# Performance work log

Hardware: AMD Instinct MI355X
Metric: run time of the kernel (lower is better)

The kernel has to match this reference:

```python
import jax, jax.numpy as jnp
import numpy as np

NEG_RATIO = 3.0           # negative_ratio
FALLBACK_NEG = 0.0        # fallback_negative_num
EPS = 1e-6                # eps
LOG_CLAMP = -100.0        # torch BCELoss clamps log to -100


def setup_inputs() -> dict:
    key = jax.random.key(0)
    k1, k2, k3 = jax.random.split(key, 3)
    shape = (32, 640, 640)  # [B, H, W] DBNet-style shrink maps
    # probabilities strictly inside (0,1)
    pred = jax.random.uniform(k1, shape, jnp.float32, 1e-4, 1.0 - 1e-4)
    gt = (jax.random.uniform(k2, shape) < 0.05).astype(jnp.float32)
    mask = (jax.random.uniform(k3, shape) < 0.9).astype(jnp.float32)
    return {"pred": pred, "gt": gt, "mask": mask}


def reference(pred, gt, mask):
    positive = gt * mask
    negative = (1.0 - gt) * mask
    # torch uses int(sum()); masks are binary so sums are integral, floor is exact
    pos_count = jnp.floor(positive.sum())
    neg_total = jnp.floor(negative.sum())
    neg_count = jnp.where(
        pos_count == 0,
        jnp.minimum(neg_total, FALLBACK_NEG),
        jnp.minimum(neg_total, jnp.floor(pos_count * NEG_RATIO)),
    )

    # BCE with torch's log clamp at -100
    log_p = jnp.maximum(jnp.log(pred), LOG_CLAMP)
    log_1mp = jnp.maximum(jnp.log1p(-pred), LOG_CLAMP)
    loss = -(gt * log_p + (1.0 - gt) * log_1mp)

    positive_sum = (loss * positive).sum()

    # hard-negative mining: take the top `neg_count` negative losses.
    # neg_count is data-dependent, so sort descending and mask by rank
    # (jit-compatible, same math as torch.topk(...).sum()).
    neg_loss = (loss * negative).reshape(-1)
    neg_sorted = -jnp.sort(-neg_loss)  # descending
    ranks = jnp.arange(neg_sorted.shape[0], dtype=jnp.float32)
    negative_sum = jnp.where(ranks < neg_count, neg_sorted, 0.0).sum()

    return (positive_sum + negative_sum) / (pos_count + neg_count + EPS)
```

## Files before the change

### kernel.cpp

```cpp
#include <hip/hip_runtime.h>
#include <math.h>


#define NBINS1 4096
#define K1_BLOCKS 1024

struct Ctrl {
  unsigned long long pos_cnt;
  unsigned long long neg_cnt;
  unsigned long long k;
  double pos_sum;
  unsigned B;
  unsigned k_rem;
};

#define LN2F 0.69314718055994530942f

__device__ __forceinline__ float neg_loss_from(float p) {
  return -fmaxf(__log2f(1.0f - p) * LN2F, -100.0f);
}
__device__ __forceinline__ float pos_loss_from(float p) {
  return -fmaxf(__log2f(p) * LN2F, -100.0f);
}

__device__ __forceinline__ double bin_mid(unsigned b) {
  return (double)__uint_as_float((b << 19) | 0x40000u);
}

extern "C" __global__ void __launch_bounds__(256)
k1_hist(const float* __restrict__ pred, const float* __restrict__ gt,
        const float* __restrict__ mask, unsigned* __restrict__ hist1,
        Ctrl* __restrict__ ctrl, int n4, int n) {
  __shared__ unsigned h[NBINS1];
  for (int i = threadIdx.x; i < NBINS1; i += blockDim.x) h[i] = 0u;
  __syncthreads();

  unsigned pc = 0, nc = 0;
  double psum = 0.0;
  const float4* p4 = (const float4*)pred;
  const float4* g4 = (const float4*)gt;
  const float4* m4 = (const float4*)mask;
  int gtid = blockIdx.x * blockDim.x + threadIdx.x;
  int stride = gridDim.x * blockDim.x;

  for (int i = gtid; i < n4; i += stride) {
    float4 pv = p4[i], gv = g4[i], mv = m4[i];
    float pa[4] = {pv.x, pv.y, pv.z, pv.w};
    float ga[4] = {gv.x, gv.y, gv.z, gv.w};
    float ma[4] = {mv.x, mv.y, mv.z, mv.w};
#pragma unroll
    for (int j = 0; j < 4; j++) {
      if (ma[j] != 0.0f) {
        if (ga[j] != 0.0f) {
          pc++; psum += (double)pos_loss_from(pa[j]);
        } else {
          nc++;
          atomicAdd(&h[__float_as_uint(neg_loss_from(pa[j])) >> 19], 1u);
        }
      }
    }
  }
  for (int i = n4 * 4 + gtid; i < n; i += stride) {
    float p = pred[i], g = gt[i], m = mask[i];
    if (m != 0.0f) {
      if (g != 0.0f) { pc++; psum += (double)pos_loss_from(p); }
      else {
        nc++;
        atomicAdd(&h[__float_as_uint(neg_loss_from(p)) >> 19], 1u);
      }
    }
  }

  unsigned long long pcl = pc, ncl = nc;
  for (int off = 32; off > 0; off >>= 1) {
    pcl += __shfl_down(pcl, off);
    ncl += __shfl_down(ncl, off);
    psum += __shfl_down(psum, off);
  }
  __shared__ unsigned long long spc[4], snc[4];
  __shared__ double sps[4];
  int wv = threadIdx.x >> 6, ln = threadIdx.x & 63;
  if (ln == 0) { spc[wv] = pcl; snc[wv] = ncl; sps[wv] = psum; }
  __syncthreads();
  if (threadIdx.x == 0) {
    unsigned long long tp = 0, tn = 0; double ts = 0.0;
    for (int w = 0; w < 4; w++) { tp += spc[w]; tn += snc[w]; ts += sps[w]; }
    atomicAdd(&ctrl->pos_cnt, tp);
    atomicAdd(&ctrl->neg_cnt, tn);
    unsafeAtomicAdd(&ctrl->pos_sum, ts);
  }
  for (int i = threadIdx.x; i < NBINS1; i += blockDim.x) {
    unsigned c = h[i];
    if (c) atomicAdd(&hist1[i], c);
  }
}

extern "C" __global__ void __launch_bounds__(256)
k5_final(const unsigned* __restrict__ hist1, Ctrl* __restrict__ ctrl,
         float* __restrict__ out) {
  const int T = 256, CH = NBINS1 / T;
  __shared__ unsigned long long sarr[T];
  __shared__ unsigned long long sk;
  __shared__ unsigned sB, skrem;
  __shared__ double sred[4];
  int t = threadIdx.x;
  int wv = t >> 6, ln = t & 63;

  unsigned cnt[CH];
  unsigned long long tot = 0;
  for (int j = 0; j < CH; j++) { cnt[j] = hist1[t * CH + j]; tot += cnt[j]; }
  sarr[t] = tot;
  if (t == 0) {
    sB = 0xFFFFFFFFu; skrem = 0u;
    unsigned long long pos = ctrl->pos_cnt, negtot = ctrl->neg_cnt;
    unsigned long long k = 0;
    if (pos > 0) {
      k = pos * 3ull;
      if (k > negtot) k = negtot;
    }
    ctrl->k = k;
    sk = k;
  }
  __syncthreads();
  for (int off = 1; off < T; off <<= 1) {
    unsigned long long v = (t + off < T) ? sarr[t + off] : 0ull;
    __syncthreads();
    sarr[t] += v;
    __syncthreads();
  }
  unsigned long long k = sk;
  if (k > 0) {
    unsigned long long above = sarr[t] - tot;
    if (above < k && sarr[t] >= k) {
      unsigned long long cum = above;
      for (int j = CH - 1; j >= 0; j--) {
        if (cum + (unsigned long long)cnt[j] >= k) {
          sB = (unsigned)(t * CH + j);
          skrem = (unsigned)(k - cum);
          break;
        }
        cum += cnt[j];
      }
    }
  }
  __syncthreads();
  unsigned B = sB;

  double s = 0.0;
  if (B != 0xFFFFFFFFu) {
    for (int j = 0; j < CH; j++) {
      unsigned bi = (unsigned)(t * CH + j);
      if (bi > B && cnt[j]) s += (double)cnt[j] * bin_mid(bi);
    }
  }
  for (int off = 32; off > 0; off >>= 1) s += __shfl_down(s, off);
  if (ln == 0) sred[wv] = s;
  __syncthreads();
  if (t == 0) {
    double neg_sum = sred[0] + sred[1] + sred[2] + sred[3];
    if (skrem > 0 && B != 0xFFFFFFFFu)
      neg_sum += (double)skrem * bin_mid(B);
    double denom = (double)ctrl->pos_cnt + (double)k + 1e-6;
    out[0] = (float)((ctrl->pos_sum + neg_sum) / denom);
  }
}

extern "C" void kernel_launch(void* const* d_in, const int* in_sizes, int n_in,
                              void* d_out, int out_size, void* d_ws, size_t ws_size,
                              hipStream_t stream) {
  const float* pred = (const float*)d_in[0];
  const float* gt   = (const float*)d_in[1];
  const float* mask = (const float*)d_in[2];
  float* out = (float*)d_out;
  int n = in_sizes[0];
  int n4 = n / 4;
  char* ws = (char*)d_ws;

  const size_t HIST1_OFF = 256;
  const size_t ZERO_BYTES = HIST1_OFF + NBINS1 * sizeof(unsigned);

  Ctrl* ctrl = (Ctrl*)ws;
  unsigned* hist1 = (unsigned*)(ws + HIST1_OFF);

  hipMemsetAsync(d_ws, 0, ZERO_BYTES, stream);
  k1_hist<<<K1_BLOCKS, 256, 0, stream>>>(pred, gt, mask, hist1, ctrl, n4, n);
  k5_final<<<1, 256, 0, stream>>>(hist1, ctrl, out);
}
```

Measured before the change: 198.1 us.

## Replace grid-stride histogram loop with one-shot blocks of two float4s per thread

Drops the fixed 1024-block grid-stride loop. It launches one block per 512 float4 groups, and each thread loads two float4 per input up front before processing them. This raises memory-level parallelism and the number of blocks in flight. The cost is far more blocks (about 6400), and each one clears and merges a 4096-bin shared histogram into global memory with atomics, which greatly increases global atomic traffic and per-block setup work. It also skips the global counter atomics when the values are zero.

```diff
diff --git a/kernel.cpp b/kernel.cpp
--- a/kernel.cpp
+++ b/kernel.cpp
@@ -3,7 +3,8 @@
 
 
 #define NBINS1 4096
-#define K1_BLOCKS 1024
+#define IPT 2
+#define E_THREADS 256
 
 struct Ctrl {
   unsigned long long pos_cnt;
@@ -27,46 +28,63 @@
   return (double)__uint_as_float((b << 19) | 0x40000u);
 }
 
-extern "C" __global__ void __launch_bounds__(256)
-k1_hist(const float* __restrict__ pred, const float* __restrict__ gt,
+extern "C" __global__ void __launch_bounds__(E_THREADS)
+e1_hist(const float* __restrict__ pred, const float* __restrict__ gt,
         const float* __restrict__ mask, unsigned* __restrict__ hist1,
         Ctrl* __restrict__ ctrl, int n4, int n) {
   __shared__ unsigned h[NBINS1];
-  for (int i = threadIdx.x; i < NBINS1; i += blockDim.x) h[i] = 0u;
-  __syncthreads();
-
-  unsigned pc = 0, nc = 0;
-  double psum = 0.0;
+  for (int i = threadIdx.x; i < NBINS1; i += E_THREADS) h[i] = 0u;
+  __syncthreads();
+
   const float4* p4 = (const float4*)pred;
   const float4* g4 = (const float4*)gt;
   const float4* m4 = (const float4*)mask;
-  int gtid = blockIdx.x * blockDim.x + threadIdx.x;
-  int stride = gridDim.x * blockDim.x;
-
-  for (int i = gtid; i < n4; i += stride) {
-    float4 pv = p4[i], gv = g4[i], mv = m4[i];
-    float pa[4] = {pv.x, pv.y, pv.z, pv.w};
-    float ga[4] = {gv.x, gv.y, gv.z, gv.w};
-    float ma[4] = {mv.x, mv.y, mv.z, mv.w};
+
+  int base = blockIdx.x * (E_THREADS * IPT) + threadIdx.x;
+  float4 pv[IPT], gv[IPT], mv[IPT];
+  bool inb[IPT];
 #pragma unroll
-    for (int j = 0; j < 4; j++) {
-      if (ma[j] != 0.0f) {
-        if (ga[j] != 0.0f) {
-          pc++; psum += (double)pos_loss_from(pa[j]);
+  for (int j = 0; j < IPT; j++) {
+    int i = base + j * E_THREADS;
+    inb[j] = (i < n4);
+    if (inb[j]) { pv[j] = p4[i]; gv[j] = g4[i]; mv[j] = m4[i]; }
+    else {
+      pv[j] = make_float4(0.5f, 0.5f, 0.5f, 0.5f);
+      gv[j] = make_float4(0.f, 0.f, 0.f, 0.f);
+      mv[j] = make_float4(0.f, 0.f, 0.f, 0.f);
+    }
+  }
+
+  unsigned pc = 0, nc = 0;
+  double psum = 0.0;
+#pragma unroll
+  for (int j = 0; j < IPT; j++) {
+    float pa[4] = {pv[j].x, pv[j].y, pv[j].z, pv[j].w};
+    float ga[4] = {gv[j].x, gv[j].y, gv[j].z, gv[j].w};
+    float ma[4] = {mv[j].x, mv[j].y, mv[j].z, mv[j].w};
+#pragma unroll
+    for (int e = 0; e < 4; e++) {
+      if (ma[e] != 0.0f) {
+        if (ga[e] != 0.0f) {
+          pc++; psum += (double)pos_loss_from(pa[e]);
         } else {
           nc++;
-          atomicAdd(&h[__float_as_uint(neg_loss_from(pa[j])) >> 19], 1u);
+          atomicAdd(&h[__float_as_uint(neg_loss_from(pa[e])) >> 19], 1u);
         }
       }
     }
   }
-  for (int i = n4 * 4 + gtid; i < n; i += stride) {
-    float p = pred[i], g = gt[i], m = mask[i];
-    if (m != 0.0f) {
-      if (g != 0.0f) { pc++; psum += (double)pos_loss_from(p); }
-      else {
-        nc++;
-        atomicAdd(&h[__float_as_uint(neg_loss_from(p)) >> 19], 1u);
+  {
+    int gtid = blockIdx.x * E_THREADS + threadIdx.x;
+    int gstride = gridDim.x * E_THREADS;
+    for (int i = n4 * 4 + gtid; i < n; i += gstride) {
+      float p = pred[i], g = gt[i], m = mask[i];
+      if (m != 0.0f) {
+        if (g != 0.0f) { pc++; psum += (double)pos_loss_from(p); }
+        else {
+          nc++;
+          atomicAdd(&h[__float_as_uint(neg_loss_from(p)) >> 19], 1u);
+        }
       }
     }
   }
@@ -85,11 +103,11 @@
   if (threadIdx.x == 0) {
     unsigned long long tp = 0, tn = 0; double ts = 0.0;
     for (int w = 0; w < 4; w++) { tp += spc[w]; tn += snc[w]; ts += sps[w]; }
-    atomicAdd(&ctrl->pos_cnt, tp);
-    atomicAdd(&ctrl->neg_cnt, tn);
-    unsafeAtomicAdd(&ctrl->pos_sum, ts);
-  }
-  for (int i = threadIdx.x; i < NBINS1; i += blockDim.x) {
+    if (tp) atomicAdd(&ctrl->pos_cnt, tp);
+    if (tn) atomicAdd(&ctrl->neg_cnt, tn);
+    if (ts != 0.0) unsafeAtomicAdd(&ctrl->pos_sum, ts);
+  }
+  for (int i = threadIdx.x; i < NBINS1; i += E_THREADS) {
     unsigned c = h[i];
     if (c) atomicAdd(&hist1[i], c);
   }
@@ -182,7 +200,10 @@
   Ctrl* ctrl = (Ctrl*)ws;
   unsigned* hist1 = (unsigned*)(ws + HIST1_OFF);
 
+  int blocks = (n4 + E_THREADS * IPT - 1) / (E_THREADS * IPT);
+  if (blocks < 1) blocks = 1;
+
   hipMemsetAsync(d_ws, 0, ZERO_BYTES, stream);
-  k1_hist<<<K1_BLOCKS, 256, 0, stream>>>(pred, gt, mask, hist1, ctrl, n4, n);
+  e1_hist<<<blocks, E_THREADS, 0, stream>>>(pred, gt, mask, hist1, ctrl, n4, n);
   k5_final<<<1, 256, 0, stream>>>(hist1, ctrl, out);
 }
```

New measurement: 361.5 us. 1.82x slower.
